# Kernel optimization log

Hardware: AMD Instinct MI355X
Metric: run time of the kernel (lower is better)

Reference implementation:

```python
import jax, jax.numpy as jnp
import numpy as np

NUM_USERS = 100000
NUM_ITEMS = 50000
N = NUM_USERS + NUM_ITEMS
EMB = 64
NNZ = 4000000
B = 4096
GAMMA = 1.0
REG_LAMBDA = 1e-4
T_END = 1.0  # Euler step size: t = [0, 1]
EPS = 1e-12


def setup_inputs() -> dict:
    key = jax.random.key(0)
    ks = jax.random.split(key, 8)
    user = jax.random.randint(ks[0], (B,), 0, NUM_USERS)
    positive = jax.random.randint(ks[1], (B,), 0, NUM_ITEMS)
    negative = jax.random.randint(ks[2], (B,), 0, NUM_ITEMS)
    adj_rows = jax.random.randint(ks[3], (NNZ,), 0, N)
    adj_cols = jax.random.randint(ks[4], (NNZ,), 0, N)
    # normalized-adjacency-like small positive values
    adj_vals = jax.random.uniform(ks[5], (NNZ,), jnp.float32) * 1e-3
    user_emb = jax.random.normal(ks[6], (NUM_USERS, EMB), jnp.float32) * 0.1
    item_emb = jax.random.normal(ks[7], (NUM_ITEMS, EMB), jnp.float32) * 0.1
    return {
        "user": user, "positive": positive, "negative": negative,
        "adj_rows": adj_rows, "adj_cols": adj_cols, "adj_vals": adj_vals,
        "user_emb": user_emb, "item_emb": item_emb,
    }


def _normalize(x):
    return x * jax.lax.rsqrt(jnp.sum(x * x, axis=-1, keepdims=True) + EPS)


def _uniform_loss(x):
    # log mean_{i<j} exp(-2 * ||xn_i - xn_j||^2), xn = L2-normalized
    xn = _normalize(x)
    sq = jnp.maximum(2.0 - 2.0 * (xn @ xn.T), 0.0)  # [B, B] pairwise squared dist
    mask = jnp.triu(jnp.ones((x.shape[0], x.shape[0]), bool), k=1)
    vals = jnp.where(mask, jnp.exp(-2.0 * sq), 0.0)
    n_pairs = x.shape[0] * (x.shape[0] - 1) / 2.0
    return jnp.log(jnp.sum(vals) / n_pairs)


def reference(user, positive, negative, adj_rows, adj_cols, adj_vals, user_emb, item_emb):
    # ego embeddings: concat user/item tables -> [N, EMB]
    x = jnp.concatenate([user_emb, item_emb], axis=0)
    # sparse spmm: ax = A @ x (COO gather + segment reduce)
    ax = jax.ops.segment_sum(adj_vals[:, None] * x[adj_cols], adj_rows, num_segments=N)
    # ODEFunc f(t, x) = A@x + e with e = x0; one Euler step z1 = x0 + t*(A@x0 + x0)
    z = x + T_END * (ax + x)
    u_all, i_all = z[:NUM_USERS], z[NUM_USERS:]
    u = u_all[user]          # [B, EMB]
    i = i_all[positive]      # [B, EMB]
    # alignment loss on normalized embeddings
    un, inn = _normalize(u), _normalize(i)
    align = jnp.mean(jnp.sum((un - inn) ** 2, axis=-1))
    # uniformity loss
    uniform = GAMMA * (_uniform_loss(u) + _uniform_loss(i)) / 2.0
    # L2 reg on ego (pre-propagation) embeddings
    ego_u = user_emb[user]
    ego_i = item_emb[positive]
    reg = REG_LAMBDA * 0.5 * (jnp.sum(ego_u ** 2) + jnp.sum(ego_i ** 2)) / B
    return jnp.stack([align, uniform, reg])
```

## Files before the change

kernel.cpp:

```cpp
#include <hip/hip_runtime.h>
#include <math.h>

#define NUSERS 100000
#define NITEMS 50000
#define NN (NUSERS + NITEMS)
#define EMB 64
#define NNZ_ 4000000
#define BB 4096
#define NSLOT (2 * BB)
#define CAP 128
#define FSTR 32
#define BMW 4688
#define EPSN 1e-12f
#define NT 32
#define NTRI 528
#define NG (NNZ_ / 4)
#define NM4 (NG / 4)


typedef __attribute__((ext_vector_type(8))) short short8v;
typedef __attribute__((ext_vector_type(16))) float f32x16;

__device__ inline float wave_reduce_sum(float v) {
  #pragma unroll
  for (int off = 32; off >= 1; off >>= 1) v += __shfl_xor(v, off, 64);
  return v;
}

__device__ inline unsigned short f2bf(float f) {
  unsigned u = __float_as_uint(f);
  unsigned r = u + 0x7fffu + ((u >> 16) & 1u);
  return (unsigned short)(r >> 16);
}

__global__ __launch_bounds__(256) void lg_init(int* map, int* fillp, unsigned* bitmap) {
  int t = blockIdx.x * blockDim.x + threadIdx.x;
  if (t < NN) map[t] = -1;
  if (t < NSLOT * FSTR) fillp[t] = 0;
  if (t < BMW) bitmap[t] = 0u;
}

__global__ __launch_bounds__(256) void lg_mark(const int* __restrict__ user,
                                               const int* __restrict__ positive,
                                               int* __restrict__ map,
                                               unsigned* __restrict__ bitmap) {
  int t = blockIdx.x * blockDim.x + threadIdx.x;
  if (t >= 2 * BB) return;
  int row = (t < BB) ? user[t] : (NUSERS + positive[t - BB]);
  atomicCAS(&map[row], -1, t);
  atomicOr(&bitmap[row >> 5], 1u << (row & 31));
}

__global__ __launch_bounds__(256) void lg_probe(const int4* __restrict__ rows4,
                                                const unsigned* __restrict__ bitmap,
                                                unsigned char* __restrict__ mask) {
  int t = blockIdx.x * 256 + threadIdx.x;
  if (t >= NG) return;
  int4 r = rows4[t];
  unsigned h = ((bitmap[r.x >> 5] >> (r.x & 31)) & 1u)
             | (((bitmap[r.y >> 5] >> (r.y & 31)) & 1u) << 1)
             | (((bitmap[r.z >> 5] >> (r.z & 31)) & 1u) << 2)
             | (((bitmap[r.w >> 5] >> (r.w & 31)) & 1u) << 3);
  mask[t] = (unsigned char)h;
}

__global__ __launch_bounds__(256) void lg_collect(const unsigned* __restrict__ mask4,
                                                  const int* __restrict__ rows,
                                                  const int* __restrict__ cols,
                                                  const float* __restrict__ vals,
                                                  const int* __restrict__ map,
                                                  int* __restrict__ fillp,
                                                  uint2* __restrict__ bins) {
  __shared__ int qk[4][1024];
  __shared__ int qn[4];
  int t = threadIdx.x;
  int lane = t & 63, w = t >> 6;
  if (lane == 0) qn[w] = 0;
  __syncthreads();
  int g = blockIdx.x * 256 + t;
  unsigned m = (g < NM4) ? mask4[g] : 0u;
  while (m) {
    int p = __ffs(m) - 1;
    m &= m - 1;
    int k = g * 16 + (p >> 3) * 4 + (p & 7);
    int pos = atomicAdd(&qn[w], 1);
    qk[w][pos] = k;
  }
  __syncthreads();
  int n = qn[w];
  for (int i = lane; i < n; i += 64) {
    int k = qk[w][i];
    int r = rows[k];
    int c = cols[k];
    float v = vals[k];
    int s = map[r];
    int pos = atomicAdd(&fillp[s * FSTR], 1);
    if (pos < CAP) bins[(size_t)s * CAP + pos] = make_uint2((unsigned)c, __float_as_uint(v));
  }
}

__global__ __launch_bounds__(256) void lg_accum(const int* __restrict__ fillp,
                                                const uint2* __restrict__ bins,
                                                const float* __restrict__ uemb,
                                                const float* __restrict__ iemb,
                                                float* __restrict__ acc) {
  int w = (blockIdx.x * blockDim.x + threadIdx.x) >> 6;
  int lane = threadIdx.x & 63;
  if (w >= NSLOT) return;
  int n = min(fillp[w * FSTR], CAP);
  const uint2* bs = bins + (size_t)w * CAP;
  float a = 0.0f;
  int k = 0;
  for (; k + 4 <= n; k += 4) {
    uint2 e0 = bs[k];
    uint2 e1 = bs[k + 1];
    uint2 e2 = bs[k + 2];
    uint2 e3 = bs[k + 3];
    int c0 = (int)e0.x; float v0 = __uint_as_float(e0.y);
    int c1 = (int)e1.x; float v1 = __uint_as_float(e1.y);
    int c2 = (int)e2.x; float v2 = __uint_as_float(e2.y);
    int c3 = (int)e3.x; float v3 = __uint_as_float(e3.y);
    const float* x0 = (c0 < NUSERS) ? uemb + (size_t)c0 * EMB : iemb + (size_t)(c0 - NUSERS) * EMB;
    const float* x1 = (c1 < NUSERS) ? uemb + (size_t)c1 * EMB : iemb + (size_t)(c1 - NUSERS) * EMB;
    const float* x2 = (c2 < NUSERS) ? uemb + (size_t)c2 * EMB : iemb + (size_t)(c2 - NUSERS) * EMB;
    const float* x3 = (c3 < NUSERS) ? uemb + (size_t)c3 * EMB : iemb + (size_t)(c3 - NUSERS) * EMB;
    float f0 = x0[lane], f1 = x1[lane], f2 = x2[lane], f3 = x3[lane];
    a = fmaf(v0, f0, a);
    a = fmaf(v1, f1, a);
    a = fmaf(v2, f2, a);
    a = fmaf(v3, f3, a);
  }
  for (; k < n; ++k) {
    uint2 e0 = bs[k];
    int c0 = (int)e0.x; float v0 = __uint_as_float(e0.y);
    const float* x0 = (c0 < NUSERS) ? uemb + (size_t)c0 * EMB : iemb + (size_t)(c0 - NUSERS) * EMB;
    a = fmaf(v0, x0[lane], a);
  }
  acc[(size_t)w * EMB + lane] = a;
}

__global__ __launch_bounds__(256) void lg_prep(const int* __restrict__ user,
                                               const int* __restrict__ positive,
                                               const float* __restrict__ uemb,
                                               const float* __restrict__ iemb,
                                               const int* __restrict__ map,
                                               const float* __restrict__ acc,
                                               unsigned short* __restrict__ zub,
                                               unsigned short* __restrict__ zib,
                                               float* __restrict__ part_align,
                                               float* __restrict__ part_reg) {
  int w = (blockIdx.x * blockDim.x + threadIdx.x) >> 6;
  int lane = threadIdx.x & 63;
  if (w >= BB) return;
  int ru = user[w];
  int pi = positive[w];
  float eu = uemb[(size_t)ru * EMB + lane];
  float ei = iemb[(size_t)pi * EMB + lane];
  int su = map[ru];
  int si = map[NUSERS + pi];
  float zul = 2.0f * eu + acc[(size_t)su * EMB + lane];
  float zil = 2.0f * ei + acc[(size_t)si * EMB + lane];
  float nu = wave_reduce_sum(zul * zul);
  float ni = wave_reduce_sum(zil * zil);
  float un = zul * rsqrtf(nu + EPSN);
  float inn = zil * rsqrtf(ni + EPSN);
  zub[(size_t)w * EMB + lane] = f2bf(un);
  zib[(size_t)w * EMB + lane] = f2bf(inn);
  float d = un - inn;
  float align_b = wave_reduce_sum(d * d);
  float reg_b = wave_reduce_sum(eu * eu + ei * ei);
  if (lane == 0) {
    part_align[w] = align_b;
    part_reg[w] = reg_b;
  }
}

__global__ __launch_bounds__(256) void lg_gram_mfma(const unsigned short* __restrict__ zub,
                                                    const unsigned short* __restrict__ zib,
                                                    float* __restrict__ gpart) {
  int L = blockIdx.x, m = blockIdx.y;
  int ib = 0, rem = L;
  while (rem >= NT - ib) { rem -= NT - ib; ++ib; }
  int jb = ib + rem;
  const unsigned short* z = (m == 0) ? zub : zib;
  __shared__ uint4 As4[1024];
  __shared__ uint4 Bs4[1024];
  __shared__ float wsum[4];
  int t = threadIdx.x;
  const uint4* srcA = (const uint4*)(z + (size_t)ib * 128 * EMB);
  const uint4* srcB = (const uint4*)(z + (size_t)jb * 128 * EMB);
  #pragma unroll
  for (int it = 0; it < 4; ++it) {
    int idx = it * 256 + t;
    int r = idx >> 3, s = idx & 7;
    int dst = r * 8 + (s ^ (r & 7));
    As4[dst] = srcA[idx];
    Bs4[dst] = srcB[idx];
  }
  __syncthreads();
  int l = t & 63, w = t >> 6;
  int wr = w >> 1, wc = w & 1;
  int lr = l & 31;
  int h = l >> 5;
  int ra0 = wr * 64 + lr;
  int ra1 = ra0 + 32;
  int rb0 = wc * 64 + lr;
  int rb1 = rb0 + 32;
  f32x16 a00 = {}, a01 = {}, a10 = {}, a11 = {};
  #pragma unroll
  for (int ks = 0; ks < 4; ++ks) {
    int seg = ks * 2 + h;
    short8v a0 = *(const short8v*)&As4[ra0 * 8 + (seg ^ (ra0 & 7))];
    short8v a1 = *(const short8v*)&As4[ra1 * 8 + (seg ^ (ra1 & 7))];
    short8v b0 = *(const short8v*)&Bs4[rb0 * 8 + (seg ^ (rb0 & 7))];
    short8v b1 = *(const short8v*)&Bs4[rb1 * 8 + (seg ^ (rb1 & 7))];
    a00 = __builtin_amdgcn_mfma_f32_32x32x16_bf16(a0, b0, a00, 0, 0, 0);
    a01 = __builtin_amdgcn_mfma_f32_32x32x16_bf16(a0, b1, a01, 0, 0, 0);
    a10 = __builtin_amdgcn_mfma_f32_32x32x16_bf16(a1, b0, a10, 0, 0, 0);
    a11 = __builtin_amdgcn_mfma_f32_32x32x16_bf16(a1, b1, a11, 0, 0, 0);
  }
  float s = 0.0f;
  #pragma unroll
  for (int e = 0; e < 16; ++e) {
    s += __expf(-2.0f * fmaxf(fmaf(-2.0f, a00[e], 2.0f), 0.0f));
    s += __expf(-2.0f * fmaxf(fmaf(-2.0f, a01[e], 2.0f), 0.0f));
    s += __expf(-2.0f * fmaxf(fmaf(-2.0f, a10[e], 2.0f), 0.0f));
    s += __expf(-2.0f * fmaxf(fmaf(-2.0f, a11[e], 2.0f), 0.0f));
  }
  s = wave_reduce_sum(s);
  if (l == 0) wsum[w] = s;
  __syncthreads();
  if (t == 0) {
    float tot = wsum[0] + wsum[1] + wsum[2] + wsum[3];
    float wgt = (ib == jb) ? 1.0f : 2.0f;
    gpart[m * NTRI + L] = wgt * tot;
  }
}

__global__ __launch_bounds__(256) void lg_final(const float* __restrict__ part_align,
                                                const float* __restrict__ part_reg,
                                                const float* __restrict__ gpart,
                                                float* __restrict__ out) {
  __shared__ float red[4][4];
  int t = threadIdx.x;
  float sa = 0.0f, sr = 0.0f, su = 0.0f, si = 0.0f;
  for (int k = t; k < 4096; k += 256) {
    sa += part_align[k];
    sr += part_reg[k];
  }
  for (int k = t; k < NTRI; k += 256) {
    su += gpart[k];
    si += gpart[NTRI + k];
  }
  sa = wave_reduce_sum(sa);
  sr = wave_reduce_sum(sr);
  su = wave_reduce_sum(su);
  si = wave_reduce_sum(si);
  if ((t & 63) == 0) {
    int wid = t >> 6;
    red[wid][0] = sa; red[wid][1] = sr; red[wid][2] = su; red[wid][3] = si;
  }
  __syncthreads();
  if (t == 0) {
    float a = 0, r = 0, Su = 0, Si = 0;
    #pragma unroll
    for (int wv = 0; wv < 4; ++wv) {
      a += red[wv][0]; r += red[wv][1]; Su += red[wv][2]; Si += red[wv][3];
    }
    float align = a / (float)BB;
    float reg = 1e-4f * 0.5f * r / (float)BB;
    float npairs = (float)BB * (float)(BB - 1) * 0.5f;
    float tri_u = (Su - (float)BB) * 0.5f;
    float tri_i = (Si - (float)BB) * 0.5f;
    float Lu = logf(tri_u / npairs);
    float Li = logf(tri_i / npairs);
    out[0] = align;
    out[1] = 0.5f * (Lu + Li);
    out[2] = reg;
  }
}

extern "C" void kernel_launch(void* const* d_in, const int* in_sizes, int n_in,
                              void* d_out, int out_size, void* d_ws, size_t ws_size,
                              hipStream_t stream) {
  const int* user = (const int*)d_in[0];
  const int* positive = (const int*)d_in[1];
  const int* adj_rows = (const int*)d_in[3];
  const int* adj_cols = (const int*)d_in[4];
  const float* adj_vals = (const float*)d_in[5];
  const float* uemb = (const float*)d_in[6];
  const float* iemb = (const float*)d_in[7];

  char* ws = (char*)d_ws;
  int* map = (int*)(ws);
  int* fillp = (int*)(ws + (1u << 20));
  uint2* bins = (uint2*)(ws + (2u << 20));
  float* acc = (float*)(ws + (10u << 20));
  unsigned short* zub = (unsigned short*)(ws + (12u << 20));
  unsigned short* zib = (unsigned short*)(ws + (12u << 20) + (512u << 10));
  float* part_align = (float*)(ws + (13u << 20));
  float* part_reg = (float*)(ws + (13u << 20) + (16u << 10));
  float* gpart = (float*)(ws + (13u << 20) + (32u << 10));
  unsigned* bitmap = (unsigned*)(ws + (13u << 20) + (64u << 10));
  unsigned char* hitmask = (unsigned char*)(ws + (14u << 20));
  float* out = (float*)d_out;

  lg_init<<<dim3(1024), dim3(256), 0, stream>>>(map, fillp, bitmap);
  lg_mark<<<dim3(32), dim3(256), 0, stream>>>(user, positive, map, bitmap);
  lg_probe<<<dim3((NG + 255) / 256), dim3(256), 0, stream>>>(
      (const int4*)adj_rows, bitmap, hitmask);
  lg_collect<<<dim3((NM4 + 255) / 256), dim3(256), 0, stream>>>(
      (const unsigned*)hitmask, adj_rows, adj_cols, adj_vals, map, fillp, bins);
  lg_accum<<<dim3(NSLOT / 4), dim3(256), 0, stream>>>(fillp, bins, uemb, iemb, acc);
  lg_prep<<<dim3(1024), dim3(256), 0, stream>>>(user, positive, uemb, iemb, map,
                                                acc, zub, zib, part_align, part_reg);
  lg_gram_mfma<<<dim3(NTRI, 2), dim3(256), 0, stream>>>(zub, zib, gpart);
  lg_final<<<dim3(1), dim3(256), 0, stream>>>(part_align, part_reg, gpart, out);
}
```

Baseline: 69.36 us.

## Fuse row-probe and edge-collect kernels into one ballot-compacted scan-bin kernel

The separate probe kernel (which wrote a per-edge hit mask to global memory) and collect kernel (which re-read that mask plus the rows array) become one kernel. Each thread loads two int4 row groups, tests them against the bitmap, and compacts hits into per-wave shared queues using ballot/popcount instead of LDS atomics. It then bins the hits directly. This removes a kernel launch, the mask write and read, and the second rows read, at the cost of a fixed grid of 2048 blocks each covering two strided groups.

```diff
diff --git a/kernel.cpp b/kernel.cpp
--- a/kernel.cpp
+++ b/kernel.cpp
@@ -15,7 +15,7 @@
 #define NT 32
 #define NTRI 528
 #define NG (NNZ_ / 4)
-#define NM4 (NG / 4)
+#define SGRID 2048
 
 
 typedef __attribute__((ext_vector_type(8))) short short8v;
@@ -51,51 +51,58 @@
   atomicOr(&bitmap[row >> 5], 1u << (row & 31));
 }
 
-__global__ __launch_bounds__(256) void lg_probe(const int4* __restrict__ rows4,
-                                                const unsigned* __restrict__ bitmap,
-                                                unsigned char* __restrict__ mask) {
-  int t = blockIdx.x * 256 + threadIdx.x;
-  if (t >= NG) return;
-  int4 r = rows4[t];
-  unsigned h = ((bitmap[r.x >> 5] >> (r.x & 31)) & 1u)
-             | (((bitmap[r.y >> 5] >> (r.y & 31)) & 1u) << 1)
-             | (((bitmap[r.z >> 5] >> (r.z & 31)) & 1u) << 2)
-             | (((bitmap[r.w >> 5] >> (r.w & 31)) & 1u) << 3);
-  mask[t] = (unsigned char)h;
-}
-
-__global__ __launch_bounds__(256) void lg_collect(const unsigned* __restrict__ mask4,
-                                                  const int* __restrict__ rows,
-                                                  const int* __restrict__ cols,
-                                                  const float* __restrict__ vals,
-                                                  const int* __restrict__ map,
-                                                  int* __restrict__ fillp,
-                                                  uint2* __restrict__ bins) {
-  __shared__ int qk[4][1024];
-  __shared__ int qn[4];
+__global__ __launch_bounds__(256) void lg_scan_bin(const int4* __restrict__ rows4,
+                                                   const int* __restrict__ cols,
+                                                   const float* __restrict__ vals,
+                                                   const unsigned* __restrict__ bitmap,
+                                                   const int* __restrict__ map,
+                                                   int* __restrict__ fillp,
+                                                   uint2* __restrict__ bins) {
+  __shared__ int qr[4][512];
+  __shared__ int qk[4][512];
   int t = threadIdx.x;
   int lane = t & 63, w = t >> 6;
-  if (lane == 0) qn[w] = 0;
-  __syncthreads();
-  int g = blockIdx.x * 256 + t;
-  unsigned m = (g < NM4) ? mask4[g] : 0u;
-  while (m) {
-    int p = __ffs(m) - 1;
-    m &= m - 1;
-    int k = g * 16 + (p >> 3) * 4 + (p & 7);
-    int pos = atomicAdd(&qn[w], 1);
-    qk[w][pos] = k;
-  }
-  __syncthreads();
-  int n = qn[w];
-  for (int i = lane; i < n; i += 64) {
-    int k = qk[w][i];
-    int r = rows[k];
-    int c = cols[k];
-    float v = vals[k];
-    int s = map[r];
+  unsigned long long lmlt = (1ull << lane) - 1ull;
+  const int STR = SGRID * 256;
+  int g0 = blockIdx.x * 256 + t;
+  int g1 = g0 + STR;
+  bool v1 = g1 < NG;
+  int4 r0 = rows4[g0];
+  int4 r1 = v1 ? rows4[g1] : make_int4(0, 0, 0, 0);
+  bool h0 = ((bitmap[r0.x >> 5] >> (r0.x & 31)) & 1u);
+  bool h1 = ((bitmap[r0.y >> 5] >> (r0.y & 31)) & 1u);
+  bool h2 = ((bitmap[r0.z >> 5] >> (r0.z & 31)) & 1u);
+  bool h3 = ((bitmap[r0.w >> 5] >> (r0.w & 31)) & 1u);
+  bool h4 = v1 && ((bitmap[r1.x >> 5] >> (r1.x & 31)) & 1u);
+  bool h5 = v1 && ((bitmap[r1.y >> 5] >> (r1.y & 31)) & 1u);
+  bool h6 = v1 && ((bitmap[r1.z >> 5] >> (r1.z & 31)) & 1u);
+  bool h7 = v1 && ((bitmap[r1.w >> 5] >> (r1.w & 31)) & 1u);
+  int k0 = g0 * 4, k1 = g1 * 4;
+  int qn = 0;
+  #define ENQ(hh, rr, kk)                                                   \
+  {                                                                         \
+    unsigned long long m = __ballot(hh);                                    \
+    if (hh) { int p = qn + (int)__popcll(m & lmlt); qr[w][p] = (rr);        \
+              qk[w][p] = (kk); }                                            \
+    qn += (int)__popcll(m);                                                 \
+  }
+  ENQ(h0, r0.x, k0 + 0)
+  ENQ(h1, r0.y, k0 + 1)
+  ENQ(h2, r0.z, k0 + 2)
+  ENQ(h3, r0.w, k0 + 3)
+  ENQ(h4, r1.x, k1 + 0)
+  ENQ(h5, r1.y, k1 + 1)
+  ENQ(h6, r1.z, k1 + 2)
+  ENQ(h7, r1.w, k1 + 3)
+  #undef ENQ
+  for (int i = lane; i < qn; i += 64) {
+    int rr = qr[w][i];
+    int kk = qk[w][i];
+    int s = map[rr];
+    int c = cols[kk];
+    float fv = vals[kk];
     int pos = atomicAdd(&fillp[s * FSTR], 1);
-    if (pos < CAP) bins[(size_t)s * CAP + pos] = make_uint2((unsigned)c, __float_as_uint(v));
+    if (pos < CAP) bins[(size_t)s * CAP + pos] = make_uint2((unsigned)c, __float_as_uint(fv));
   }
 }
 
@@ -302,15 +309,12 @@
   float* part_reg = (float*)(ws + (13u << 20) + (16u << 10));
   float* gpart = (float*)(ws + (13u << 20) + (32u << 10));
   unsigned* bitmap = (unsigned*)(ws + (13u << 20) + (64u << 10));
-  unsigned char* hitmask = (unsigned char*)(ws + (14u << 20));
   float* out = (float*)d_out;
 
   lg_init<<<dim3(1024), dim3(256), 0, stream>>>(map, fillp, bitmap);
   lg_mark<<<dim3(32), dim3(256), 0, stream>>>(user, positive, map, bitmap);
-  lg_probe<<<dim3((NG + 255) / 256), dim3(256), 0, stream>>>(
-      (const int4*)adj_rows, bitmap, hitmask);
-  lg_collect<<<dim3((NM4 + 255) / 256), dim3(256), 0, stream>>>(
-      (const unsigned*)hitmask, adj_rows, adj_cols, adj_vals, map, fillp, bins);
+  lg_scan_bin<<<dim3(SGRID), dim3(256), 0, stream>>>(
+      (const int4*)adj_rows, adj_cols, adj_vals, bitmap, map, fillp, bins);
   lg_accum<<<dim3(NSLOT / 4), dim3(256), 0, stream>>>(fillp, bins, uemb, iemb, acc);
   lg_prep<<<dim3(1024), dim3(256), 0, stream>>>(user, positive, uemb, iemb, map,
                                                 acc, zub, zib, part_align, part_reg);
```

Result: faster. 60.86 us (-12.3%).
